# Optimization experiments

Measured on AMD Instinct MI355X. Metric: run time of the kernel, lower is better.

The kernel has to match this reference:

```python
import jax, jax.numpy as jnp
import numpy as np

B, H, W = 2, 128, 128
MID = 64            # mid_channels
DG = 16             # deform_groups
MAX_RES = 10.0      # max_residue_magnitude
CIN_OFF = 3 * MID + 4   # 196: cat(extra_feat, flow_1, flow_2)
COFF = DG * 27          # 432: o1 + o2 + mask, each DG*9


def setup_inputs() -> dict:
    key = jax.random.key(0)
    ks = jax.random.split(key, 9)
    return {
        "extra_feat": jax.random.normal(ks[0], (B, 3 * MID, H, W), jnp.float32),
        "flow_1": jax.random.normal(ks[1], (B, 2, H, W), jnp.float32) * 2.0,
        "flow_2": jax.random.normal(ks[2], (B, 2, H, W), jnp.float32) * 2.0,
        "feat_prop": jax.random.normal(ks[3], (B, MID, H, W), jnp.float32),
        "feat_n2": jax.random.normal(ks[4], (B, MID, H, W), jnp.float32),
        "w_off": jax.random.normal(ks[5], (COFF, CIN_OFF, 3, 3), jnp.float32) * 0.02,
        "b_off": jax.random.normal(ks[6], (COFF,), jnp.float32) * 0.02,
        "dc_weight": jax.random.normal(ks[7], (MID, 2 * MID, 3, 3), jnp.float32) * 0.05,
        "dc_bias": jax.random.normal(ks[8], (MID,), jnp.float32) * 0.05,
    }


def _conv3x3(x, w, b):
    y = jax.lax.conv_general_dilated(
        x, w, window_strides=(1, 1), padding=((1, 1), (1, 1)),
        dimension_numbers=("NCHW", "OIHW", "NCHW"))
    return y + b[None, :, None, None]


def _deform_conv2d(inp, offset, mask, weight, bias):
    # inp: [B, Cin, H, W]; offset: [B, 2*DG*9, H, W] (per group, per kernel pos: (dy, dx));
    # mask: [B, DG*9, H, W]; weight: [Cout, Cin, 3, 3]; stride=1, pad=1, dil=1.
    Bb, Cin, Hi, Wi = inp.shape
    K = 9
    cg = Cin // DG
    Ho, Wo = Hi, Wi
    ki = jnp.repeat(jnp.arange(3), 3)  # kernel row index per flat k (row-major)
    kj = jnp.tile(jnp.arange(3), 3)
    base_y = (jnp.arange(Ho) - 1)[None, :, None] + ki[:, None, None]  # [K, Ho, 1]
    base_x = (jnp.arange(Wo) - 1)[None, None, :] + kj[:, None, None]  # [K, 1, Wo]
    off = offset.reshape(Bb, DG, K, 2, Ho, Wo)
    py = base_y[None, None] + off[:, :, :, 0]  # [B, DG, K, Ho, Wo]
    px = base_x[None, None] + off[:, :, :, 1]
    y0 = jnp.floor(py)
    x0 = jnp.floor(px)
    inp_g = inp.reshape(Bb, DG, cg, Hi * Wi)
    acc = jnp.zeros((Bb, DG, cg, K, Ho, Wo), inp.dtype)
    for dy in (0.0, 1.0):
        for dx in (0.0, 1.0):
            yc = y0 + dy
            xc = x0 + dx
            wgt = (1.0 - jnp.abs(py - yc)) * (1.0 - jnp.abs(px - xc))
            valid = (yc >= 0) & (yc < Hi) & (xc >= 0) & (xc < Wi)
            idx = (jnp.clip(yc, 0, Hi - 1) * Wi + jnp.clip(xc, 0, Wi - 1)).astype(jnp.int32)
            idx = jnp.broadcast_to(idx.reshape(Bb, DG, 1, K * Ho * Wo), (Bb, DG, cg, K * Ho * Wo))
            g = jnp.take_along_axis(inp_g, idx, axis=3).reshape(Bb, DG, cg, K, Ho, Wo)
            acc = acc + g * (wgt * valid)[:, :, None]
    sm = acc * mask.reshape(Bb, DG, 1, K, Ho, Wo)  # modulated samples
    wr = weight.reshape(weight.shape[0], DG, cg, K)
    out = jnp.einsum("bgckhw,ogck->bohw", sm, wr) + bias[None, :, None, None]
    return out


def reference(extra_feat, flow_1, flow_2, feat_prop, feat_n2, w_off, b_off, dc_weight, dc_bias):
    x = jnp.concatenate([extra_feat, flow_1, flow_2], axis=1)
    out = _conv3x3(x, w_off, b_off)
    o1, o2, m = jnp.split(out, 3, axis=1)  # each [B, DG*9, H, W]
    offset = MAX_RES * jnp.tanh(jnp.concatenate([o1, o2], axis=1))
    rep = DG * 3 * 3 // 2  # 72
    f1 = jnp.tile(flow_1[:, ::-1], (1, rep, 1, 1))  # flip(1): (dx,dy)->(dy,dx)
    f2 = jnp.tile(flow_2[:, ::-1], (1, rep, 1, 1))
    half = offset.shape[1] // 2
    offset = jnp.concatenate([offset[:, :half] + f1, offset[:, half:] + f2], axis=1)
    mask = jax.nn.sigmoid(m)
    inp = jnp.concatenate([feat_prop, feat_n2], axis=1)
    return _deform_conv2d(inp, offset, mask, dc_weight, dc_bias)
```

## Files before the change

kernel.cpp:

```cpp
#include <hip/hip_runtime.h>
#include <math.h>

#define Hh 128
#define Ww 128
#define HW (128*128)
#define CIN_OFF 196
#define COFF 432

typedef _Float16 half8 __attribute__((ext_vector_type(8)));
typedef _Float16 half4 __attribute__((ext_vector_type(4)));
typedef _Float16 half2v __attribute__((ext_vector_type(2)));
typedef float f32x4 __attribute__((ext_vector_type(4)));

static __device__ __forceinline__ half8 splat8(float v) {
  _Float16 h = (_Float16)v;
  half8 r = {h, h, h, h, h, h, h, h};
  return r;
}

__global__ __launch_bounds__(256) void k_prep_all(
    const float* __restrict__ dcw, const float* __restrict__ w_off,
    const float* __restrict__ fp, const float* __restrict__ fn2,
    _Float16* __restrict__ wH, _Float16* __restrict__ BpT, _Float16* __restrict__ Bt,
    _Float16* __restrict__ featT) {
  const int bid = blockIdx.x;
  if (bid < 3375) {
    const int idx = bid * 256 + (int)threadIdx.x;
    if (idx < 73728) {
      const int co = idx / 1152;
      const int j  = idx - co * 1152;
      const int k  = j >> 7;
      const int ci = j & 127;
      wH[idx] = (_Float16)dcw[(co * 128 + ci) * 9 + k];
    } else if (idx < 73728 + 774144) {
      const int j  = idx - 73728;
      const int c  = j & 7;
      const int n  = (j >> 3) % 448;
      const int sl = (j >> 3) / 448;
      const int l4 = sl & 3;
      const int s  = sl >> 2;
      const int t  = s / 6;
      const int cg = s - t * 6;
      const int ci = cg * 32 + l4 * 8 + c;
      BpT[j] = (_Float16)((n < COFF) ? w_off[((size_t)n * CIN_OFF + ci) * 9 + t] : 0.f);
    } else {
      const int j = idx - 73728 - 774144;
      const int c = j & 3;
      const int n = (j >> 2) % 448;
      const int t = (j >> 2) / 448;
      Bt[j] = (_Float16)((n < COFF) ? w_off[((size_t)n * CIN_OFF + 192 + c) * 9 + t] : 0.f);
    }
  } else {
    const int t = (bid - 3375) * 256 + (int)threadIdx.x;
    const int b = t >> 14;
    const int hw = t & 16383;
#pragma unroll
    for (int g = 0; g < 16; ++g) {
      const float* src = (g < 8) ? fp : fn2;
      const int ch0 = (g & 7) * 8;
      half8 v;
#pragma unroll
      for (int c = 0; c < 8; ++c)
        v[c] = (_Float16)src[(size_t)(b * 64 + ch0 + c) * HW + hw];
      *(half8*)(featT + (((size_t)(b * 16 + g)) * HW + hw) * 8) = v;
    }
  }
}

__global__ __launch_bounds__(512, 4) void k_offconv_mfma(
    const float* __restrict__ extra, const float* __restrict__ f1, const float* __restrict__ f2,
    const _Float16* __restrict__ BpT, const _Float16* __restrict__ Bt,
    const float* __restrict__ b_off,
    _Float16* __restrict__ off_pm, _Float16* __restrict__ mask_pm) {
  __shared__ __align__(16) _Float16 smA[3 * 66 * 192];
  __shared__ __align__(16) _Float16 smT[3 * 66 * 4];
  const int wt   = blockIdx.x;
  const int h    = blockIdx.y;
  const int b    = blockIdx.z;
  const int w0   = wt * 64;
  const int tid  = (int)threadIdx.x;
  const int lane = tid & 63;
  const int wid  = tid >> 6;
  const int wm   = wid & 1;
  const int wn   = (wid >> 1) & 3;
  const int m_base = wm * 32;
  const int n_base = wn * 112;
  const int l15 = lane & 15;
  const int l4  = lane >> 4;

#pragma unroll 3
  for (int it = 0; it < 9; ++it) {
    const int J   = tid + 512 * it;
    const int p2a = J & 15;
    const int qa  = (J >> 4) & 3;
    const int R   = J >> 6;
    const int r   = R / 24;
    const int rem = R - 24 * r;
    const int qh  = rem & 3;
    const int p2h = rem >> 2;
    const int q   = qa + 4 * qh;
    const int p2  = p2a + 16 * p2h;
    const int ci  = 2 * p2;
    const int gh  = h - 1 + r;
    float4 va = {0.f, 0.f, 0.f, 0.f}, vb = va;
    if ((unsigned)gh < (unsigned)Hh) {
      const float* xp = extra + (size_t)(b * 192 + ci) * HW + gh * Ww + w0 + 4 * q;
      va = *(const float4*)xp;
      vb = *(const float4*)(xp + HW);
    }
    const float av[4] = {va.x, va.y, va.z, va.w};
    const float bv[4] = {vb.x, vb.y, vb.z, vb.w};
    const int biw = p2 >> 2;
#pragma unroll
    for (int i = 0; i < 4; ++i) {
      const int px = 1 + 4 * q + i;
      const int sw = ((biw & 24) | ((biw & 7) ^ (px & 7))) << 3;
      half2v pk; pk[0] = (_Float16)av[i]; pk[1] = (_Float16)bv[i];
      *(half2v*)(smA + (r * 66 + px) * 192 + sw + (ci & 7)) = pk;
    }
  }
  if (tid < 96) {
    const int r   = tid >> 5;
    const int rem = tid & 31;
    const int pt  = rem >> 4;
    const int q   = rem & 15;
    const int gh  = h - 1 + r;
    float4 va = {0.f, 0.f, 0.f, 0.f}, vb = va;
    if ((unsigned)gh < (unsigned)Hh) {
      const float* xp = (pt ? f2 : f1) + (size_t)(b * 2) * HW + gh * Ww + w0 + 4 * q;
      va = *(const float4*)xp;
      vb = *(const float4*)(xp + HW);
    }
    const float av[4] = {va.x, va.y, va.z, va.w};
    const float bv[4] = {vb.x, vb.y, vb.z, vb.w};
#pragma unroll
    for (int i = 0; i < 4; ++i) {
      const int px = 1 + 4 * q + i;
      half2v pk; pk[0] = (_Float16)av[i]; pk[1] = (_Float16)bv[i];
      *(half2v*)(smT + (r * 66 + px) * 4 + 2 * pt) = pk;
    }
  }
  for (int z = tid; z < 588; z += 512) {
    if (z < 576) {
      const int r    = z / 192;
      const int rem  = z - r * 192;
      const int side = rem / 96;
      const int p2   = rem - side * 96;
      const int px   = side ? 65 : 0;
      const int col  = w0 - 1 + px;
      const int ci   = 2 * p2;
      const int gh   = h - 1 + r;
      float s0 = 0.f, s1 = 0.f;
      if ((unsigned)gh < (unsigned)Hh && (unsigned)col < (unsigned)Ww) {
        const float* xp = extra + (size_t)(b * 192 + ci) * HW + gh * Ww + col;
        s0 = xp[0];
        s1 = xp[HW];
      }
      const int biw = p2 >> 2;
      const int sw = ((biw & 24) | ((biw & 7) ^ (px & 7))) << 3;
      half2v pk; pk[0] = (_Float16)s0; pk[1] = (_Float16)s1;
      *(half2v*)(smA + (r * 66 + px) * 192 + sw + (ci & 7)) = pk;
    } else {
      const int t2   = z - 576;
      const int r    = t2 >> 2;
      const int rem  = t2 & 3;
      const int side = rem >> 1;
      const int pt   = rem & 1;
      const int px   = side ? 65 : 0;
      const int col  = w0 - 1 + px;
      const int gh   = h - 1 + r;
      float s0 = 0.f, s1 = 0.f;
      if ((unsigned)gh < (unsigned)Hh && (unsigned)col < (unsigned)Ww) {
        const float* xp = (pt ? f2 : f1) + (size_t)(b * 2) * HW + gh * Ww + col;
        s0 = xp[0];
        s1 = xp[HW];
      }
      half2v pk; pk[0] = (_Float16)s0; pk[1] = (_Float16)s1;
      *(half2v*)(smT + (r * 66 + px) * 4 + 2 * pt) = pk;
    }
  }
  __syncthreads();

  f32x4 acc[2][7];
#pragma unroll
  for (int i = 0; i < 2; ++i)
#pragma unroll
    for (int j = 0; j < 7; ++j) acc[i][j] = (f32x4){0.f, 0.f, 0.f, 0.f};

  const bool lz = (l4 == 0);
#pragma unroll 3
  for (int t = 0; t < 9; ++t) {
    const int ki = t / 3;
    const int kj = t - 3 * ki;
#pragma unroll
    for (int cg = 0; cg < 6; ++cg) {
      const int s4 = ((t * 6 + cg) * 4 + l4) * 448;
      half8 bf[7];
#pragma unroll
      for (int f = 0; f < 7; ++f)
        bf[f] = *(const half8*)(BpT + (size_t)(s4 + n_base + f * 16 + l15) * 8);
      half8 af[2];
#pragma unroll
      for (int mf = 0; mf < 2; ++mf) {
        const int px = m_base + mf * 16 + l15 + kj;
        const int bi = cg * 4 + l4;
        af[mf] = *(const half8*)(smA + (ki * 66 + px) * 192 +
                                 (((bi & 24) | ((bi & 7) ^ (px & 7))) << 3));
      }
#pragma unroll
      for (int mf = 0; mf < 2; ++mf)
#pragma unroll
        for (int f = 0; f < 7; ++f)
          acc[mf][f] = __builtin_amdgcn_mfma_f32_16x16x32_f16(af[mf], bf[f], acc[mf][f], 0, 0, 0);
    }
    half8 aft[2];
#pragma unroll
    for (int mf = 0; mf < 2; ++mf) {
      const int px = m_base + mf * 16 + l15 + kj;
      const half4 tv = *(const half4*)(smT + (ki * 66 + px) * 4);
      half8 a = {0, 0, 0, 0, 0, 0, 0, 0};
      if (lz) { a[0] = tv[0]; a[1] = tv[1]; a[2] = tv[2]; a[3] = tv[3]; }
      aft[mf] = a;
    }
#pragma unroll
    for (int f = 0; f < 7; ++f) {
      const half4 wv = *(const half4*)(Bt + (size_t)(t * 448 + n_base + f * 16 + l15) * 4);
      half8 bb = {0, 0, 0, 0, 0, 0, 0, 0};
      if (lz) { bb[0] = wv[0]; bb[1] = wv[1]; bb[2] = wv[2]; bb[3] = wv[3]; }
#pragma unroll
      for (int mf = 0; mf < 2; ++mf)
        acc[mf][f] = __builtin_amdgcn_mfma_f32_16x16x32_f16(aft[mf], bb, acc[mf][f], 0, 0, 0);
    }
  }

  __syncthreads();
  _Float16* so = smA;
  const int hw0 = h * Ww + w0;
#pragma unroll
  for (int f = 0; f < 7; ++f) {
    const int n = n_base + f * 16 + l15;
    const float bias = (n < COFF) ? b_off[n] : 0.f;
    const bool isOff = (n < 288);
    const float* fl = (n < 144) ? f1 : f2;
    const size_t fladd = (size_t)(b * 2 + ((n & 1) ^ 1)) * HW + hw0;
#pragma unroll
    for (int mf = 0; mf < 2; ++mf) {
#pragma unroll
      for (int rr = 0; rr < 4; ++rr) {
        const int px = m_base + mf * 16 + l4 * 4 + rr;
        const float v = acc[mf][f][rr] + bias;
        float val;
        if (isOff) {
          const float e = __expf(2.f * v);
          val = 10.f * (1.f - 2.f / (e + 1.f)) + fl[fladd + px];
        } else {
          val = 1.f / (1.f + __expf(-v));
        }
        so[px * 456 + n] = (_Float16)val;
      }
    }
  }
  __syncthreads();
  for (int T = tid; T < 2304; T += 512) {
    const int px = T / 36, c = T - px * 36;
    const half8 v = *(const half8*)(so + px * 456 + c * 8);
    *(half8*)(off_pm + ((size_t)b * HW + hw0 + px) * 288 + c * 8) = v;
  }
  for (int T = tid; T < 1152; T += 512) {
    const int px = T / 18, c = T - px * 18;
    const half8 v = *(const half8*)(so + px * 456 + 288 + c * 8);
    *(half8*)(mask_pm + ((size_t)b * HW + hw0 + px) * 144 + c * 8) = v;
  }
}

__global__ __launch_bounds__(256, 4) void k_deform2(
    const _Float16* __restrict__ featT, const _Float16* __restrict__ off_pm,
    const _Float16* __restrict__ mask_pm, const _Float16* __restrict__ wH,
    const float* __restrict__ dcb, float* __restrict__ out) {
  __shared__ __align__(16) char smem[16 * 1160 * 2];
  _Float16* sm = (_Float16*)smem;
  float* red = (float*)smem;
  const int w0  = blockIdx.x * 16;
  const int h   = blockIdx.y;
  const int b   = blockIdx.z;
  const int tid = (int)threadIdx.x;
  const int lane = tid & 63, wid = tid >> 6;
  const int l15 = lane & 15, l4 = lane >> 4;

  half2v offv[9];
  _Float16 mkv[9];
#pragma unroll
  for (int i = 0; i < 9; ++i) {
    const int p   = tid + i * 256;
    const int pix = p / 144;
    const int r   = p - pix * 144;
    const int w   = w0 + pix;
    const int hw  = h * Ww + w;
    offv[i] = *(const half2v*)(off_pm + ((size_t)b * HW + hw) * 288 + 2 * r);
    mkv[i]  = mask_pm[((size_t)b * HW + hw) * 144 + r];
  }
#pragma unroll
  for (int i = 0; i < 9; ++i) {
    const int p   = tid + i * 256;
    const int pix = p / 144;
    const int r   = p - pix * 144;
    const int g   = r / 9;
    const int k   = r - g * 9;
    const int w   = w0 + pix;
    const float mk = (float)mkv[i];
    const int ki = (k >= 6) ? 2 : (k >= 3 ? 1 : 0);
    const int kj = k - 3 * ki;
    const float py = (float)(h - 1 + ki) + (float)offv[i][0];
    const float px = (float)(w - 1 + kj) + (float)offv[i][1];
    const float y0f = floorf(py), x0f = floorf(px);
    const int y0 = (int)y0f, x0 = (int)x0f;
    const float ly = py - y0f, lx = px - x0f;
    const float hy = 1.f - ly, hx = 1.f - lx;
    const int y1 = y0 + 1, x1 = x0 + 1;
    const bool vy0 = (unsigned)y0 < (unsigned)Hh, vy1 = (unsigned)y1 < (unsigned)Hh;
    const bool vx0 = (unsigned)x0 < (unsigned)Ww, vx1 = (unsigned)x1 < (unsigned)Ww;
    const float w00 = (vy0 && vx0) ? hy * hx : 0.f;
    const float w01 = (vy0 && vx1) ? hy * lx : 0.f;
    const float w10 = (vy1 && vx0) ? ly * hx : 0.f;
    const float w11 = (vy1 && vx1) ? ly * lx : 0.f;
    const int cy0 = min(max(y0, 0), Hh - 1), cy1 = min(max(y1, 0), Hh - 1);
    const int cx0 = min(max(x0, 0), Ww - 1), cx1 = min(max(x1, 0), Ww - 1);
    const _Float16* gbase = featT + ((size_t)(b * 16 + g) * HW) * 8;
    const half8 s00 = *(const half8*)(gbase + (cy0 * Ww + cx0) * 8);
    const half8 s01 = *(const half8*)(gbase + (cy0 * Ww + cx1) * 8);
    const half8 s10 = *(const half8*)(gbase + (cy1 * Ww + cx0) * 8);
    const half8 s11 = *(const half8*)(gbase + (cy1 * Ww + cx1) * 8);
    half8 v = s00 * splat8(w00) + s01 * splat8(w01) + s10 * splat8(w10) + s11 * splat8(w11);
    v = v * splat8(mk);
    const int swz = (g ^ (k & 7)) << 3;
    *(half8*)(sm + pix * 1160 + k * 128 + swz) = v;
  }
  __syncthreads();

  f32x4 acc[4];
#pragma unroll
  for (int nf = 0; nf < 4; ++nf) acc[nf] = (f32x4){0.f, 0.f, 0.f, 0.f};
#pragma unroll
  for (int j = 0; j < 9; ++j) {
    const int s  = wid * 9 + j;
    const int k  = s >> 2;
    const int cg = s & 3;
    const int gidx = cg * 4 + l4;
    const half8 af = *(const half8*)(sm + l15 * 1160 + k * 128 + ((gidx ^ (k & 7)) << 3));
    const int koff = s * 32 + l4 * 8;
#pragma unroll
    for (int nf = 0; nf < 4; ++nf) {
      const half8 bf = *(const half8*)(wH + (nf * 16 + l15) * 1152 + koff);
      acc[nf] = __builtin_amdgcn_mfma_f32_16x16x32_f16(af, bf, acc[nf], 0, 0, 0);
    }
  }
  __syncthreads();
#pragma unroll
  for (int nf = 0; nf < 4; ++nf)
#pragma unroll
    for (int rr = 0; rr < 4; ++rr)
      red[(wid * 16 + l4 * 4 + rr) * 66 + nf * 16 + l15] = acc[nf][rr];
  __syncthreads();

  const int m  = tid & 15;
  const int ng = tid >> 4;
#pragma unroll
  for (int i = 0; i < 4; ++i) {
    const int n = ng + 16 * i;
    float val = red[(0 * 16 + m) * 66 + n] + red[(1 * 16 + m) * 66 + n] +
                red[(2 * 16 + m) * 66 + n] + red[(3 * 16 + m) * 66 + n];
    out[(size_t)(b * 64 + n) * HW + h * Ww + w0 + m] = val + dcb[n];
  }
}

extern "C" void kernel_launch(void* const* d_in, const int* in_sizes, int n_in,
                              void* d_out, int out_size, void* d_ws, size_t ws_size,
                              hipStream_t stream) {
  const float* extra = (const float*)d_in[0];
  const float* f1    = (const float*)d_in[1];
  const float* f2    = (const float*)d_in[2];
  const float* fp    = (const float*)d_in[3];
  const float* fn2   = (const float*)d_in[4];
  const float* w_off = (const float*)d_in[5];
  const float* b_off = (const float*)d_in[6];
  const float* dcw   = (const float*)d_in[7];
  const float* dcb   = (const float*)d_in[8];
  float* out = (float*)d_out;

  _Float16* off_pm  = (_Float16*)d_ws;
  _Float16* mask_pm = off_pm + (size_t)2 * 288 * HW;
  _Float16* featT   = mask_pm + (size_t)2 * 144 * HW;
  _Float16* BpT     = featT + (size_t)2 * 128 * HW;
  _Float16* Bt      = BpT + 774144;
  _Float16* wH      = Bt + 16128;

  hipLaunchKernelGGL(k_prep_all, dim3(3503), dim3(256), 0, stream,
                     dcw, w_off, fp, fn2, wH, BpT, Bt, featT);
  hipLaunchKernelGGL(k_offconv_mfma, dim3(2, 128, 2), dim3(512), 0, stream,
                     extra, f1, f2, BpT, Bt, b_off, off_pm, mask_pm);
  hipLaunchKernelGGL(k_deform2, dim3(8, 128, 2), dim3(256), 0, stream,
                     featT, off_pm, mask_pm, wH, dcb, out);
}
```

Measured before the change: 186.2 us.

## Swizzle blocks across XCDs, widen deform tiles, reorganize weight prep, add MFMA priority

Flattens the grids of the offset-conv and deform kernels and remaps block IDs so neighbouring rows land on the same XCD, improving L2 locality. The deform kernel now handles 32 pixels per block with 512 threads, split into two pixel halves times four K quarters. The offset-weight prep now has each thread read nine contiguous taps, which cuts the block count and improves read coalescing. s_setprio is raised around the MFMA bursts. Trade-offs: fewer, larger deform blocks with twice the LDS per block, and the swizzle assumes the grid size divides evenly by 8.

```diff
diff --git a/kernel.cpp b/kernel.cpp
--- a/kernel.cpp
+++ b/kernel.cpp
@@ -16,6 +16,11 @@
   _Float16 h = (_Float16)v;
   half8 r = {h, h, h, h, h, h, h, h};
   return r;
+}
+
+static __device__ __forceinline__ int xcd_swz(int bid, int nwg) {
+  const int q = nwg >> 3;
+  return (bid & 7) * q + (bid >> 3);
 }
 
 __global__ __launch_bounds__(256) void k_prep_all(
@@ -24,34 +29,36 @@
     _Float16* __restrict__ wH, _Float16* __restrict__ BpT, _Float16* __restrict__ Bt,
     _Float16* __restrict__ featT) {
   const int bid = blockIdx.x;
-  if (bid < 3375) {
+  if (bid < 288) {
     const int idx = bid * 256 + (int)threadIdx.x;
-    if (idx < 73728) {
-      const int co = idx / 1152;
-      const int j  = idx - co * 1152;
-      const int k  = j >> 7;
-      const int ci = j & 127;
-      wH[idx] = (_Float16)dcw[(co * 128 + ci) * 9 + k];
-    } else if (idx < 73728 + 774144) {
-      const int j  = idx - 73728;
-      const int c  = j & 7;
-      const int n  = (j >> 3) % 448;
-      const int sl = (j >> 3) / 448;
-      const int l4 = sl & 3;
-      const int s  = sl >> 2;
-      const int t  = s / 6;
-      const int cg = s - t * 6;
-      const int ci = cg * 32 + l4 * 8 + c;
-      BpT[j] = (_Float16)((n < COFF) ? w_off[((size_t)n * CIN_OFF + ci) * 9 + t] : 0.f);
-    } else {
-      const int j = idx - 73728 - 774144;
+    const int co = idx / 1152;
+    const int j  = idx - co * 1152;
+    const int k  = j >> 7;
+    const int ci = j & 127;
+    wH[idx] = (_Float16)dcw[(co * 128 + ci) * 9 + k];
+  } else if (bid < 624) {
+    const int idx = (bid - 288) * 256 + (int)threadIdx.x;
+    const int n  = idx / 192;
+    const int ci = idx - n * 192;
+    const int l4 = (ci >> 3) & 3;
+    const int c  = ci & 7;
+    const int cg = ci >> 5;
+    const float* src = w_off + ((size_t)n * CIN_OFF + ci) * 9;
+#pragma unroll
+    for (int t = 0; t < 9; ++t) {
+      const float v = (n < COFF) ? src[t] : 0.f;
+      BpT[((size_t)((t * 6 + cg) * 4 + l4) * 448 + n) * 8 + c] = (_Float16)v;
+    }
+  } else if (bid < 687) {
+    const int j = (bid - 624) * 256 + (int)threadIdx.x;
+    if (j < 16128) {
       const int c = j & 3;
       const int n = (j >> 2) % 448;
       const int t = (j >> 2) / 448;
       Bt[j] = (_Float16)((n < COFF) ? w_off[((size_t)n * CIN_OFF + 192 + c) * 9 + t] : 0.f);
     }
   } else {
-    const int t = (bid - 3375) * 256 + (int)threadIdx.x;
+    const int t = (bid - 687) * 256 + (int)threadIdx.x;
     const int b = t >> 14;
     const int hw = t & 16383;
 #pragma unroll
@@ -74,9 +81,10 @@
     _Float16* __restrict__ off_pm, _Float16* __restrict__ mask_pm) {
   __shared__ __align__(16) _Float16 smA[3 * 66 * 192];
   __shared__ __align__(16) _Float16 smT[3 * 66 * 4];
-  const int wt   = blockIdx.x;
-  const int h    = blockIdx.y;
-  const int b    = blockIdx.z;
+  const int nb   = xcd_swz((int)blockIdx.x, 512);
+  const int wt   = nb & 1;
+  const int h    = (nb >> 1) & 127;
+  const int b    = nb >> 8;
   const int w0   = wt * 64;
   const int tid  = (int)threadIdx.x;
   const int lane = tid & 63;
@@ -207,11 +215,13 @@
         af[mf] = *(const half8*)(smA + (ki * 66 + px) * 192 +
                                  (((bi & 24) | ((bi & 7) ^ (px & 7))) << 3));
       }
+      __builtin_amdgcn_s_setprio(1);
 #pragma unroll
       for (int mf = 0; mf < 2; ++mf)
 #pragma unroll
         for (int f = 0; f < 7; ++f)
           acc[mf][f] = __builtin_amdgcn_mfma_f32_16x16x32_f16(af[mf], bf[f], acc[mf][f], 0, 0, 0);
+      __builtin_amdgcn_s_setprio(0);
     }
     half8 aft[2];
 #pragma unroll
@@ -227,9 +237,11 @@
       const half4 wv = *(const half4*)(Bt + (size_t)(t * 448 + n_base + f * 16 + l15) * 4);
       half8 bb = {0, 0, 0, 0, 0, 0, 0, 0};
       if (lz) { bb[0] = wv[0]; bb[1] = wv[1]; bb[2] = wv[2]; bb[3] = wv[3]; }
+      __builtin_amdgcn_s_setprio(1);
 #pragma unroll
       for (int mf = 0; mf < 2; ++mf)
         acc[mf][f] = __builtin_amdgcn_mfma_f32_16x16x32_f16(aft[mf], bb, acc[mf][f], 0, 0, 0);
+      __builtin_amdgcn_s_setprio(0);
     }
   }
 
@@ -273,16 +285,17 @@
   }
 }
 
-__global__ __launch_bounds__(256, 4) void k_deform2(
+__global__ __launch_bounds__(512, 2) void k_deform2(
     const _Float16* __restrict__ featT, const _Float16* __restrict__ off_pm,
     const _Float16* __restrict__ mask_pm, const _Float16* __restrict__ wH,
     const float* __restrict__ dcb, float* __restrict__ out) {
-  __shared__ __align__(16) char smem[16 * 1160 * 2];
+  __shared__ __align__(16) char smem[32 * 1160 * 2];
   _Float16* sm = (_Float16*)smem;
   float* red = (float*)smem;
-  const int w0  = blockIdx.x * 16;
-  const int h   = blockIdx.y;
-  const int b   = blockIdx.z;
+  const int nb  = xcd_swz((int)blockIdx.x, 1024);
+  const int w0  = (nb & 3) * 32;
+  const int h   = (nb >> 2) & 127;
+  const int b   = nb >> 9;
   const int tid = (int)threadIdx.x;
   const int lane = tid & 63, wid = tid >> 6;
   const int l15 = lane & 15, l4 = lane >> 4;
@@ -291,7 +304,7 @@
   _Float16 mkv[9];
 #pragma unroll
   for (int i = 0; i < 9; ++i) {
-    const int p   = tid + i * 256;
+    const int p   = tid + i * 512;
     const int pix = p / 144;
     const int r   = p - pix * 144;
     const int w   = w0 + pix;
@@ -301,7 +314,7 @@
   }
 #pragma unroll
   for (int i = 0; i < 9; ++i) {
-    const int p   = tid + i * 256;
+    const int p   = tid + i * 512;
     const int pix = p / 144;
     const int r   = p - pix * 144;
     const int g   = r / 9;
@@ -337,39 +350,46 @@
   }
   __syncthreads();
 
+  const int mh = wid & 1;
+  const int kq = wid >> 1;
   f32x4 acc[4];
 #pragma unroll
   for (int nf = 0; nf < 4; ++nf) acc[nf] = (f32x4){0.f, 0.f, 0.f, 0.f};
 #pragma unroll
   for (int j = 0; j < 9; ++j) {
-    const int s  = wid * 9 + j;
+    const int s  = kq * 9 + j;
     const int k  = s >> 2;
     const int cg = s & 3;
     const int gidx = cg * 4 + l4;
-    const half8 af = *(const half8*)(sm + l15 * 1160 + k * 128 + ((gidx ^ (k & 7)) << 3));
+    const half8 af = *(const half8*)(sm + (mh * 16 + l15) * 1160 + k * 128 +
+                                     ((gidx ^ (k & 7)) << 3));
     const int koff = s * 32 + l4 * 8;
+    __builtin_amdgcn_s_setprio(1);
 #pragma unroll
     for (int nf = 0; nf < 4; ++nf) {
       const half8 bf = *(const half8*)(wH + (nf * 16 + l15) * 1152 + koff);
       acc[nf] = __builtin_amdgcn_mfma_f32_16x16x32_f16(af, bf, acc[nf], 0, 0, 0);
     }
+    __builtin_amdgcn_s_setprio(0);
   }
   __syncthreads();
 #pragma unroll
   for (int nf = 0; nf < 4; ++nf)
 #pragma unroll
     for (int rr = 0; rr < 4; ++rr)
-      red[(wid * 16 + l4 * 4 + rr) * 66 + nf * 16 + l15] = acc[nf][rr];
-  __syncthreads();
-
-  const int m  = tid & 15;
-  const int ng = tid >> 4;
-#pragma unroll
-  for (int i = 0; i < 4; ++i) {
-    const int n = ng + 16 * i;
-    float val = red[(0 * 16 + m) * 66 + n] + red[(1 * 16 + m) * 66 + n] +
-                red[(2 * 16 + m) * 66 + n] + red[(3 * 16 + m) * 66 + n];
-    out[(size_t)(b * 64 + n) * HW + h * Ww + w0 + m] = val + dcb[n];
+      red[((mh * 4 + kq) * 16 + l4 * 4 + rr) * 66 + nf * 16 + l15] = acc[nf][rr];
+  __syncthreads();
+
+  for (int T = tid; T < 2048; T += 512) {
+    const int px2 = T & 31;
+    const int n   = T >> 5;
+    const int mhr = px2 >> 4;
+    const int pxl = px2 & 15;
+    float val = red[((mhr * 4 + 0) * 16 + pxl) * 66 + n] +
+                red[((mhr * 4 + 1) * 16 + pxl) * 66 + n] +
+                red[((mhr * 4 + 2) * 16 + pxl) * 66 + n] +
+                red[((mhr * 4 + 3) * 16 + pxl) * 66 + n];
+    out[(size_t)(b * 64 + n) * HW + h * Ww + w0 + px2] = val + dcb[n];
   }
 }
 
@@ -394,10 +414,10 @@
   _Float16* Bt      = BpT + 774144;
   _Float16* wH      = Bt + 16128;
 
-  hipLaunchKernelGGL(k_prep_all, dim3(3503), dim3(256), 0, stream,
+  hipLaunchKernelGGL(k_prep_all, dim3(815), dim3(256), 0, stream,
                      dcw, w_off, fp, fn2, wH, BpT, Bt, featT);
-  hipLaunchKernelGGL(k_offconv_mfma, dim3(2, 128, 2), dim3(512), 0, stream,
+  hipLaunchKernelGGL(k_offconv_mfma, dim3(512), dim3(512), 0, stream,
                      extra, f1, f2, BpT, Bt, b_off, off_pm, mask_pm);
-  hipLaunchKernelGGL(k_deform2, dim3(8, 128, 2), dim3(256), 0, stream,
+  hipLaunchKernelGGL(k_deform2, dim3(1024), dim3(512), 0, stream,
                      featT, off_pm, mask_pm, wH, dcb, out);
 }
```

Measured after the change: 170.7 us. 1.09x faster.
